# Kernel optimization log

Hardware: AMD Instinct MI355X
Metric: run time of the kernel (lower is better)

Reference implementation:

```python
import jax, jax.numpy as jnp
import numpy as np

GROUPS = 32
HEADS = 8
EPS = 1e-5

def setup_inputs() -> dict:
    key = jax.random.key(0)
    ks = jax.random.split(key, 5)
    C = 512
    x = jax.random.normal(ks[0], (8, C, 32, 32), dtype=jnp.float32)
    gn_w = jnp.ones((C,), dtype=jnp.float32)
    gn_b = jnp.zeros((C,), dtype=jnp.float32)
    qkv_w = jax.random.normal(ks[1], (3 * C, C), dtype=jnp.float32) * 0.02
    qkv_b = jnp.zeros((3 * C,), dtype=jnp.float32)
    proj_w = jax.random.normal(ks[2], (C, C), dtype=jnp.float32) * 0.02
    proj_b = jnp.zeros((C,), dtype=jnp.float32)
    return {"x": x, "gn_w": gn_w, "gn_b": gn_b, "qkv_w": qkv_w,
            "qkv_b": qkv_b, "proj_w": proj_w, "proj_b": proj_b}

def reference(x, gn_w, gn_b, qkv_w, qkv_b, proj_w, proj_b):
    B, C, H, W = x.shape
    d = C // HEADS
    # GroupNorm(32, C)
    xg = x.reshape(B, GROUPS, C // GROUPS, H, W)
    mean = xg.mean(axis=(2, 3, 4), keepdims=True)
    var = xg.var(axis=(2, 3, 4), keepdims=True)
    h = ((xg - mean) * jax.lax.rsqrt(var + EPS)).reshape(B, C, H, W)
    h = h * gn_w[None, :, None, None] + gn_b[None, :, None, None]
    # 1x1 conv QKV == channel matmul
    qkv = jnp.einsum('bchw,oc->bohw', h, qkv_w) + qkv_b[None, :, None, None]
    qkv = qkv.reshape(B, 3, HEADS, d, H * W)
    q, k, v = qkv[:, 0], qkv[:, 1], qkv[:, 2]  # [B, heads, d, HW]
    scale = d ** (-0.5)
    # weight[b,h,q,k] = sum_d q[b,h,d,q] * k[b,h,d,k] * scale
    attn = jax.nn.softmax(jnp.einsum('bhdq,bhdk->bhqk', q, k) * scale, axis=-1)
    # out[b,h,d,q] = sum_k v[b,h,d,k] * attn[b,h,q,k]
    out = jnp.einsum('bhdk,bhqk->bhdq', v, attn).reshape(B, C, H, W)
    out = jnp.einsum('bchw,oc->bohw', out, proj_w) + proj_b[None, :, None, None]
    return out + x
```

## Files before the change

kernel.cpp:

```cpp
#include <hip/hip_runtime.h>
#include <math.h>

#define B_    8
#define C_    512
#define HW_   1024
#define O3_   1536
#define HEADS_ 8
#define D_    64
#define G_    32
#define CPG_  16
#define EPS_  1e-5f
#define M_TOT 8192

#define QSCALE (0.125f * 1.44269504088896f)

typedef __bf16 bf16x8 __attribute__((ext_vector_type(8)));
typedef __bf16 bf16x4 __attribute__((ext_vector_type(4)));
typedef float  f32x4  __attribute__((ext_vector_type(4)));

__device__ __forceinline__ void async_copy16(void* lds, const void* g) {
  __builtin_amdgcn_global_load_lds(
      (const __attribute__((address_space(1))) unsigned int*)g,
      (__attribute__((address_space(3))) unsigned int*)lds, 16, 0, 0);
}

__global__ __launch_bounds__(1024) void k_gn(const float* __restrict__ x,
                                             const float* __restrict__ gw,
                                             const float* __restrict__ gb,
                                             __bf16* __restrict__ h,
                                             const float* __restrict__ qw,
                                             const float* __restrict__ pw,
                                             __bf16* __restrict__ qwb,
                                             __bf16* __restrict__ pwb) {
  __shared__ float red[34];
  __shared__ __bf16 T[16 * 1032];
  int tid = threadIdx.x;
  if (blockIdx.x >= B_ * G_) {
    int i0 = (blockIdx.x - B_ * G_) * 1024 + tid;
    for (int i = i0; i < O3_ * C_ / 4; i += 64 * 1024) {
      float4 v = ((const float4*)qw)[i];
      bf16x4 o = {(__bf16)v.x, (__bf16)v.y, (__bf16)v.z, (__bf16)v.w};
      ((bf16x4*)qwb)[i] = o;
    }
    for (int i = i0; i < C_ * C_ / 4; i += 64 * 1024) {
      float4 v = ((const float4*)pw)[i];
      bf16x4 o = {(__bf16)v.x, (__bf16)v.y, (__bf16)v.z, (__bf16)v.w};
      ((bf16x4*)pwb)[i] = o;
    }
    return;
  }
  int bg = blockIdx.x;
  int b = bg >> 5, g = bg & 31;
  const float4* xg4 = (const float4*)(x + ((size_t)(b * C_) + g * CPG_) * HW_);

  float s = 0.f, ss = 0.f;
  for (int i = tid; i < CPG_ * HW_ / 4; i += 1024) {
    float4 v = xg4[i];
    s += v.x + v.y + v.z + v.w;
    ss += v.x * v.x + v.y * v.y + v.z * v.z + v.w * v.w;
  }
  for (int off = 32; off > 0; off >>= 1) {
    s  += __shfl_down(s, off, 64);
    ss += __shfl_down(ss, off, 64);
  }
  int wv = tid >> 6;
  if ((tid & 63) == 0) { red[wv] = s; red[16 + wv] = ss; }
  __syncthreads();
  if (tid == 0) {
    float S = 0.f, SS = 0.f;
#pragma unroll
    for (int i = 0; i < 16; i++) { S += red[i]; SS += red[16 + i]; }
    float mean = S / (float)(CPG_ * HW_);
    float var  = SS / (float)(CPG_ * HW_) - mean * mean;
    red[32] = mean;
    red[33] = rsqrtf(var + EPS_);
  }
  __syncthreads();
  float mean = red[32], rstd = red[33];

  for (int i = tid; i < CPG_ * HW_ / 4; i += 1024) {
    int c = i >> 8;
    int hw4 = (i & 255) * 4;
    float ga = gw[g * CPG_ + c], be = gb[g * CPG_ + c];
    float4 v = xg4[i];
    bf16x4 pk;
    pk[0] = (__bf16)((v.x - mean) * rstd * ga + be);
    pk[1] = (__bf16)((v.y - mean) * rstd * ga + be);
    pk[2] = (__bf16)((v.z - mean) * rstd * ga + be);
    pk[3] = (__bf16)((v.w - mean) * rstd * ga + be);
    *(bf16x4*)(&T[c * 1032 + hw4]) = pk;
  }
  __syncthreads();

  __bf16* hb = h + (size_t)b * HW_ * C_ + g * CPG_;
  for (int j = tid; j < 2 * HW_; j += 1024) {
    int hw = j >> 1, c8 = (j & 1) * 8;
    bf16x8 v;
#pragma unroll
    for (int jj = 0; jj < 8; jj++) v[jj] = T[(c8 + jj) * 1032 + hw];
    *(bf16x8*)(hb + (size_t)hw * C_ + c8) = v;
  }
}

#define BKQ 32
__global__ __launch_bounds__(256, 3) void k_qkv(const __bf16* __restrict__ h,
                                                const __bf16* __restrict__ w,
                                                const float* __restrict__ bias,
                                                __bf16* __restrict__ y,
                                                __bf16* __restrict__ vT) {
  __shared__ __align__(16) __bf16 As[2][128 * BKQ];
  __shared__ __align__(16) __bf16 Bs[2][128 * BKQ];
  int m0 = blockIdx.x * 128, n0 = blockIdx.y * 128;
  int t = threadIdx.x;
  int lane = t & 63, l16 = lane & 15, quad = lane >> 4;
  int wv = t >> 6;
  int wm = (wv >> 1) * 64, wn = (wv & 1) * 64;

  int rsub = lane >> 2;
  int chunk = (lane & 3) ^ (rsub & 3);
  const __bf16* ag = h + (size_t)(m0 + wv * 32 + rsub) * C_ + chunk * 8;
  const __bf16* bg = w + (size_t)(n0 + wv * 32 + rsub) * C_ + chunk * 8;
  int sw = l16 & 3;

  auto stage = [&](int k0, int bi) {
    __bf16* la = As[bi] + wv * 1024 + lane * 8;
    __bf16* lb = Bs[bi] + wv * 1024 + lane * 8;
#pragma unroll
    for (int s = 0; s < 2; s++) {
      async_copy16(la + s * 512, ag + (size_t)(s * 16) * C_ + k0);
      async_copy16(lb + s * 512, bg + (size_t)(s * 16) * C_ + k0);
    }
  };

  f32x4 acc[4][4];
#pragma unroll
  for (int i = 0; i < 4; i++)
#pragma unroll
    for (int j = 0; j < 4; j++) acc[i][j] = f32x4{0.f, 0.f, 0.f, 0.f};

  stage(0, 0);
  stage(1 * BKQ, 1);
  for (int kk = 0; kk < 16; kk++) {
    int bi = kk & 1;
    if (kk < 15)
      asm volatile("s_waitcnt vmcnt(4)\n\ts_barrier" ::: "memory");
    else
      asm volatile("s_waitcnt vmcnt(0)\n\ts_barrier" ::: "memory");
    const __bf16* as = As[bi];
    const __bf16* bs = Bs[bi];
    bf16x8 af[4], bf[4];
#pragma unroll
    for (int i = 0; i < 4; i++) {
      af[i] = *(const bf16x8*)(as + (wm + i * 16 + l16) * BKQ + (quad ^ sw) * 8);
      bf[i] = *(const bf16x8*)(bs + (wn + i * 16 + l16) * BKQ + (quad ^ sw) * 8);
    }
    asm volatile("s_waitcnt lgkmcnt(0)\n\ts_barrier" ::: "memory");
    if (kk < 14) stage((kk + 2) * BKQ, bi);
    __builtin_amdgcn_s_setprio(1);
#pragma unroll
    for (int i = 0; i < 4; i++)
#pragma unroll
      for (int j = 0; j < 4; j++)
        acc[i][j] = __builtin_amdgcn_mfma_f32_16x16x32_bf16(af[i], bf[j],
                                                            acc[i][j], 0, 0, 0);
    __builtin_amdgcn_s_setprio(0);
  }

  if (n0 >= 2 * C_) {
    int bb = m0 >> 10;
    int tokBase = (m0 & 1023) + wm + quad * 4;
#pragma unroll
    for (int j = 0; j < 4; j++) {
      int n = n0 + wn + j * 16 + l16;
      int c = n - 2 * C_;
      float bv = bias[n];
      __bf16* vrow = vT + ((size_t)(bb * C_) + c) * HW_;
#pragma unroll
      for (int i = 0; i < 4; i++) {
        bf16x4 pk;
#pragma unroll
        for (int r = 0; r < 4; r++) pk[r] = (__bf16)(acc[i][j][r] + bv);
        *(bf16x4*)(vrow + tokBase + i * 16) = pk;
      }
    }
  } else {
    float sc = (n0 < C_) ? QSCALE : 1.0f;
#pragma unroll
    for (int j = 0; j < 4; j++) {
      int n = n0 + wn + j * 16 + l16;
      float bv = bias[n];
#pragma unroll
      for (int i = 0; i < 4; i++)
#pragma unroll
        for (int r = 0; r < 4; r++) {
          int m = m0 + wm + i * 16 + quad * 4 + r;
          y[(size_t)m * O3_ + n] = (__bf16)((acc[i][j][r] + bv) * sc);
        }
    }
  }
}

__global__ __launch_bounds__(256) void k_attn(const __bf16* __restrict__ y,
                                              const __bf16* __restrict__ vT,
                                              __bf16* __restrict__ ao) {
  __shared__ __align__(16) __bf16 Ks[2][128 * 64];
  __shared__ __align__(16) __bf16 Vt[2][64 * 128];
  __shared__ __align__(16) __bf16 Pp[4][32 * 36];
  int hd = blockIdx.x, b = blockIdx.y, qt = blockIdx.z;
  int t = threadIdx.x;
  int wv = t >> 6, lane = t & 63, l16 = lane & 15, quad = lane >> 4;
  int q0 = qt * 128 + wv * 32;

  const __bf16* base = y + (size_t)(b * HW_) * O3_ + hd * D_;
  const __bf16* kg = base + C_;
  const __bf16* vtg = vT + ((size_t)(b * C_) + hd * D_) * HW_;

  bf16x8 qb[2][2];
#pragma unroll
  for (int qg = 0; qg < 2; qg++)
#pragma unroll
    for (int dh = 0; dh < 2; dh++)
      qb[qg][dh] = *(const bf16x8*)(base + (size_t)(q0 + qg * 16 + l16) * O3_ +
                                    dh * 32 + quad * 8);

  int kRowSub = lane >> 3;
  int kChunk = (lane & 7) ^ (kRowSub & 7);

  auto stage = [&](int kt, int bi) {
#pragma unroll
    for (int s = 0; s < 4; s++) {
      int row = wv * 32 + s * 8 + kRowSub;
      async_copy16(&Ks[bi][(wv * 32 + s * 8) * 64 + lane * 8],
                   kg + (size_t)(kt + row) * O3_ + kChunk * 8);
    }
#pragma unroll
    for (int s = 0; s < 4; s++) {
      int row = wv * 16 + s * 4 + (lane >> 4);
      int c2 = (lane & 15) ^ (row & 15);
      async_copy16(&Vt[bi][(wv * 16 + s * 4) * 128 + lane * 8],
                   vtg + (size_t)row * HW_ + kt + c2 * 8);
    }
  };

  float l_run[2] = {0.f, 0.f};
  f32x4 o_acc[4][2];
#pragma unroll
  for (int dt = 0; dt < 4; dt++)
#pragma unroll
    for (int qg = 0; qg < 2; qg++) o_acc[dt][qg] = f32x4{0.f, 0.f, 0.f, 0.f};

  stage(0, 0);

  for (int step = 0; step < 8; step++) {
    int bi = step & 1;
    asm volatile("s_waitcnt vmcnt(0)\n\ts_barrier" ::: "memory");
    if (step < 7) stage((step + 1) * 128, bi ^ 1);

    const __bf16* ks = Ks[bi];
    const __bf16* vs = Vt[bi];
#pragma unroll
    for (int kh = 0; kh < 4; kh++) {
      f32x4 st[2][2];
      __builtin_amdgcn_s_setprio(1);
#pragma unroll
      for (int tti = 0; tti < 2; tti++) {
        int row = (kh * 2 + tti) * 16 + l16;
        bf16x8 ka0 = *(const bf16x8*)(&ks[row * 64 + ((quad) ^ (l16 & 7)) * 8]);
        bf16x8 ka1 = *(const bf16x8*)(&ks[row * 64 + ((4 + quad) ^ (l16 & 7)) * 8]);
        f32x4 z = {0.f, 0.f, 0.f, 0.f};
        st[tti][0] = __builtin_amdgcn_mfma_f32_16x16x32_bf16(ka0, qb[0][0], z, 0, 0, 0);
        st[tti][0] = __builtin_amdgcn_mfma_f32_16x16x32_bf16(ka1, qb[0][1], st[tti][0], 0, 0, 0);
        st[tti][1] = __builtin_amdgcn_mfma_f32_16x16x32_bf16(ka0, qb[1][0], z, 0, 0, 0);
        st[tti][1] = __builtin_amdgcn_mfma_f32_16x16x32_bf16(ka1, qb[1][1], st[tti][1], 0, 0, 0);
      }
      __builtin_amdgcn_s_setprio(0);
#pragma unroll
      for (int qg = 0; qg < 2; qg++) {
        float rs = 0.f;
#pragma unroll
        for (int tti = 0; tti < 2; tti++)
#pragma unroll
          for (int r = 0; r < 4; r++) {
            float e = __builtin_amdgcn_exp2f(st[tti][qg][r]);
            st[tti][qg][r] = e;
            rs += e;
          }
        l_run[qg] += rs;
      }
#pragma unroll
      for (int qg = 0; qg < 2; qg++)
#pragma unroll
        for (int tti = 0; tti < 2; tti++) {
          bf16x4 pk;
#pragma unroll
          for (int r = 0; r < 4; r++) pk[r] = (__bf16)st[tti][qg][r];
          *(bf16x4*)(&Pp[wv][(qg * 16 + l16) * 36 + tti * 16 + quad * 4]) = pk;
        }
      asm volatile("s_waitcnt lgkmcnt(0)" ::: "memory");
      bf16x8 pb0 = *(const bf16x8*)(&Pp[wv][l16 * 36 + quad * 8]);
      bf16x8 pb1 = *(const bf16x8*)(&Pp[wv][(16 + l16) * 36 + quad * 8]);
      __builtin_amdgcn_s_setprio(1);
#pragma unroll
      for (int dt = 0; dt < 4; dt++) {
        int vpos = ((kh * 4 + quad) ^ l16) * 8;
        bf16x8 va = *(const bf16x8*)(&vs[(dt * 16 + l16) * 128 + vpos]);
        o_acc[dt][0] = __builtin_amdgcn_mfma_f32_16x16x32_bf16(va, pb0, o_acc[dt][0], 0, 0, 0);
        o_acc[dt][1] = __builtin_amdgcn_mfma_f32_16x16x32_bf16(va, pb1, o_acc[dt][1], 0, 0, 0);
      }
      __builtin_amdgcn_s_setprio(0);
    }
  }

#pragma unroll
  for (int qg = 0; qg < 2; qg++) {
    l_run[qg] += __shfl_xor(l_run[qg], 16, 64);
    l_run[qg] += __shfl_xor(l_run[qg], 32, 64);
  }
  float inv0 = 1.f / l_run[0], inv1 = 1.f / l_run[1];

#pragma unroll
  for (int dt = 0; dt < 4; dt++) {
    bf16x4 p0, p1;
#pragma unroll
    for (int r = 0; r < 4; r++) {
      p0[r] = (__bf16)(o_acc[dt][0][r] * inv0);
      p1[r] = (__bf16)(o_acc[dt][1][r] * inv1);
    }
    int ch = hd * D_ + dt * 16 + quad * 4;
    *(bf16x4*)(ao + (size_t)(b * HW_ + q0 + l16) * C_ + ch) = p0;
    *(bf16x4*)(ao + (size_t)(b * HW_ + q0 + 16 + l16) * C_ + ch) = p1;
  }
}

#define BK 64
__global__ __launch_bounds__(256) void k_proj(const __bf16* __restrict__ ao,
                                              const __bf16* __restrict__ w,
                                              const float* __restrict__ bias,
                                              const float* __restrict__ x,
                                              float* __restrict__ out) {
  __shared__ __align__(16) __bf16 As[2][128 * BK];
  __shared__ __align__(16) __bf16 Bs[2][64 * BK];
  int n0 = blockIdx.x * 64, m0 = blockIdx.y * 128;
  int t = threadIdx.x;
  int lane = t & 63, l16 = lane & 15, quad = lane >> 4;
  int wv = t >> 6;
  int wm = (wv >> 1) * 64, wn = (wv & 1) * 32;

  int rsub = lane >> 3;
  int chunk = (lane & 7) ^ rsub;
  const __bf16* ag = w + (size_t)(m0 + wv * 32 + rsub) * C_ + chunk * 8;
  const __bf16* bg = ao + (size_t)(n0 + wv * 16 + rsub) * C_ + chunk * 8;
  int sw = l16 & 7;

  auto stage = [&](int k0, int bi) {
    __bf16* la = As[bi] + wv * 2048 + lane * 8;
    __bf16* lb = Bs[bi] + wv * 1024 + lane * 8;
#pragma unroll
    for (int s = 0; s < 4; s++)
      async_copy16(la + s * 512, ag + (size_t)(s * 8) * C_ + k0);
#pragma unroll
    for (int s = 0; s < 2; s++)
      async_copy16(lb + s * 512, bg + (size_t)(s * 8) * C_ + k0);
  };

  f32x4 acc[4][2];
#pragma unroll
  for (int i = 0; i < 4; i++)
#pragma unroll
    for (int j = 0; j < 2; j++) acc[i][j] = f32x4{0.f, 0.f, 0.f, 0.f};

  stage(0, 0);
  stage(1 * BK, 1);
  for (int kk = 0; kk < 8; kk++) {
    int bi = kk & 1;
    if (kk < 7)
      asm volatile("s_waitcnt vmcnt(6)\n\ts_barrier" ::: "memory");
    else
      asm volatile("s_waitcnt vmcnt(0)\n\ts_barrier" ::: "memory");
    const __bf16* as = As[bi];
    const __bf16* bs = Bs[bi];
    bf16x8 af[2][4], bf[2][2];
#pragma unroll
    for (int hh = 0; hh < 2; hh++) {
#pragma unroll
      for (int i = 0; i < 4; i++)
        af[hh][i] = *(const bf16x8*)(as + (wm + i * 16 + l16) * BK +
                                     ((hh * 4 + quad) ^ sw) * 8);
#pragma unroll
      for (int j = 0; j < 2; j++)
        bf[hh][j] = *(const bf16x8*)(bs + (wn + j * 16 + l16) * BK +
                                     ((hh * 4 + quad) ^ sw) * 8);
    }
    asm volatile("s_waitcnt lgkmcnt(0)\n\ts_barrier" ::: "memory");
    if (kk < 6) stage((kk + 2) * BK, bi);
    __builtin_amdgcn_s_setprio(1);
#pragma unroll
    for (int hh = 0; hh < 2; hh++)
#pragma unroll
      for (int i = 0; i < 4; i++)
#pragma unroll
        for (int j = 0; j < 2; j++)
          acc[i][j] = __builtin_amdgcn_mfma_f32_16x16x32_bf16(af[hh][i], bf[hh][j],
                                                              acc[i][j], 0, 0, 0);
    __builtin_amdgcn_s_setprio(0);
  }

  int bb = n0 >> 10;
#pragma unroll
  for (int i = 0; i < 4; i++)
#pragma unroll
    for (int r = 0; r < 4; r++) {
      int o = m0 + wm + i * 16 + quad * 4 + r;
      float bv = bias[o];
#pragma unroll
      for (int j = 0; j < 2; j++) {
        int n = n0 + wn + j * 16 + l16;
        int hw = n & 1023;
        size_t idx = ((size_t)(bb * C_ + o)) * HW_ + hw;
        out[idx] = acc[i][j][r] + bv + x[idx];
      }
    }
}

extern "C" void kernel_launch(void* const* d_in, const int* in_sizes, int n_in,
                              void* d_out, int out_size, void* d_ws, size_t ws_size,
                              hipStream_t stream) {
  const float* x      = (const float*)d_in[0];
  const float* gn_w   = (const float*)d_in[1];
  const float* gn_b   = (const float*)d_in[2];
  const float* qkv_w  = (const float*)d_in[3];
  const float* qkv_b  = (const float*)d_in[4];
  const float* proj_w = (const float*)d_in[5];
  const float* proj_b = (const float*)d_in[6];
  float* out = (float*)d_out;

  char* ws = (char*)d_ws;
  __bf16* h   = (__bf16*)(ws);
  __bf16* qwb = (__bf16*)(ws + 8388608);
  __bf16* pwb = (__bf16*)(ws + 8388608 + 1572864);
  __bf16* yq  = (__bf16*)(ws + 8388608 + 1572864 + 524288);
  __bf16* ao  = (__bf16*)(ws + 8388608 + 1572864 + 524288 + 25165824);
  __bf16* vT  = (__bf16*)(ws + 8388608 + 1572864 + 524288 + 25165824 + 8388608);

  k_gn  <<<B_ * G_ + 64, 1024, 0, stream>>>(x, gn_w, gn_b, h,
                                            qkv_w, proj_w, qwb, pwb);
  k_qkv <<<dim3(M_TOT / 128, O3_ / 128, 1), 256, 0, stream>>>(h, qwb, qkv_b, yq, vT);
  k_attn<<<dim3(HEADS_, B_, 8), 256, 0, stream>>>(yq, vT, ao);
  k_proj<<<dim3(M_TOT / 64, C_ / 128, 1), 256, 0, stream>>>(ao, pwb, proj_b, x, out);
  (void)in_sizes; (void)n_in; (void)out_size; (void)ws_size;
}
```

Baseline: 141.7 us.

## Enlarge QKV GEMM tiles to 256x256 with BK=64 and 8 waves

Rewrites the QKV projection GEMM to use 256x256 block tiles with 512 threads and a K-step of 64, using an 8-wide XOR swizzle and split LDS fragment loads inside each step. Each wave now computes a 128x64 subtile, which raises arithmetic intensity per LDS/global load and halves the number of barrier iterations. The trade-off is far fewer blocks (192 vs 768), which may underfill the GPU's CUs, plus higher register and LDS pressure (128KB LDS double-buffered).

```diff
diff --git a/kernel.cpp b/kernel.cpp
--- a/kernel.cpp
+++ b/kernel.cpp
@@ -102,66 +102,84 @@
   }
 }
 
-#define BKQ 32
-__global__ __launch_bounds__(256, 3) void k_qkv(const __bf16* __restrict__ h,
+#define BKW 64
+__global__ __launch_bounds__(512, 2) void k_qkv(const __bf16* __restrict__ h,
                                                 const __bf16* __restrict__ w,
                                                 const float* __restrict__ bias,
                                                 __bf16* __restrict__ y,
                                                 __bf16* __restrict__ vT) {
-  __shared__ __align__(16) __bf16 As[2][128 * BKQ];
-  __shared__ __align__(16) __bf16 Bs[2][128 * BKQ];
-  int m0 = blockIdx.x * 128, n0 = blockIdx.y * 128;
+  __shared__ __align__(16) __bf16 As[2][256 * BKW];
+  __shared__ __align__(16) __bf16 Bs[2][256 * BKW];
+  int m0 = blockIdx.x * 256, n0 = blockIdx.y * 256;
   int t = threadIdx.x;
   int lane = t & 63, l16 = lane & 15, quad = lane >> 4;
   int wv = t >> 6;
-  int wm = (wv >> 1) * 64, wn = (wv & 1) * 64;
-
-  int rsub = lane >> 2;
-  int chunk = (lane & 3) ^ (rsub & 3);
+  int wm = (wv >> 2) * 128, wn = (wv & 3) * 64;
+
+  int rsub = lane >> 3;
+  int chunk = (lane & 7) ^ rsub;
   const __bf16* ag = h + (size_t)(m0 + wv * 32 + rsub) * C_ + chunk * 8;
   const __bf16* bg = w + (size_t)(n0 + wv * 32 + rsub) * C_ + chunk * 8;
-  int sw = l16 & 3;
+  int sw = l16 & 7;
 
   auto stage = [&](int k0, int bi) {
-    __bf16* la = As[bi] + wv * 1024 + lane * 8;
-    __bf16* lb = Bs[bi] + wv * 1024 + lane * 8;
-#pragma unroll
-    for (int s = 0; s < 2; s++) {
-      async_copy16(la + s * 512, ag + (size_t)(s * 16) * C_ + k0);
-      async_copy16(lb + s * 512, bg + (size_t)(s * 16) * C_ + k0);
+    __bf16* la = As[bi] + wv * 32 * BKW + lane * 8;
+    __bf16* lb = Bs[bi] + wv * 32 * BKW + lane * 8;
+#pragma unroll
+    for (int s = 0; s < 4; s++) {
+      async_copy16(la + s * 8 * BKW, ag + (size_t)(s * 8) * C_ + k0);
+      async_copy16(lb + s * 8 * BKW, bg + (size_t)(s * 8) * C_ + k0);
     }
   };
 
-  f32x4 acc[4][4];
-#pragma unroll
-  for (int i = 0; i < 4; i++)
+  f32x4 acc[8][4];
+#pragma unroll
+  for (int i = 0; i < 8; i++)
 #pragma unroll
     for (int j = 0; j < 4; j++) acc[i][j] = f32x4{0.f, 0.f, 0.f, 0.f};
 
   stage(0, 0);
-  stage(1 * BKQ, 1);
-  for (int kk = 0; kk < 16; kk++) {
+  stage(BKW, 1);
+  for (int kk = 0; kk < 8; kk++) {
     int bi = kk & 1;
-    if (kk < 15)
-      asm volatile("s_waitcnt vmcnt(4)\n\ts_barrier" ::: "memory");
+    if (kk < 7)
+      asm volatile("s_waitcnt vmcnt(8)\n\ts_barrier" ::: "memory");
     else
       asm volatile("s_waitcnt vmcnt(0)\n\ts_barrier" ::: "memory");
     const __bf16* as = As[bi];
     const __bf16* bs = Bs[bi];
-    bf16x8 af[4], bf[4];
-#pragma unroll
-    for (int i = 0; i < 4; i++) {
-      af[i] = *(const bf16x8*)(as + (wm + i * 16 + l16) * BKQ + (quad ^ sw) * 8);
-      bf[i] = *(const bf16x8*)(bs + (wn + i * 16 + l16) * BKQ + (quad ^ sw) * 8);
-    }
+
+    bf16x8 af[8], bfr[4];
+#pragma unroll
+    for (int i = 0; i < 8; i++)
+      af[i] = *(const bf16x8*)(as + (wm + i * 16 + l16) * BKW + (quad ^ sw) * 8);
+#pragma unroll
+    for (int j = 0; j < 4; j++)
+      bfr[j] = *(const bf16x8*)(bs + (wn + j * 16 + l16) * BKW + (quad ^ sw) * 8);
+    __builtin_amdgcn_s_setprio(1);
+#pragma unroll
+    for (int i = 0; i < 8; i++)
+#pragma unroll
+      for (int j = 0; j < 4; j++)
+        acc[i][j] = __builtin_amdgcn_mfma_f32_16x16x32_bf16(af[i], bfr[j],
+                                                            acc[i][j], 0, 0, 0);
+    __builtin_amdgcn_s_setprio(0);
+#pragma unroll
+    for (int i = 0; i < 8; i++)
+      af[i] = *(const bf16x8*)(as + (wm + i * 16 + l16) * BKW +
+                               ((4 + quad) ^ sw) * 8);
+#pragma unroll
+    for (int j = 0; j < 4; j++)
+      bfr[j] = *(const bf16x8*)(bs + (wn + j * 16 + l16) * BKW +
+                                ((4 + quad) ^ sw) * 8);
     asm volatile("s_waitcnt lgkmcnt(0)\n\ts_barrier" ::: "memory");
-    if (kk < 14) stage((kk + 2) * BKQ, bi);
+    if (kk < 6) stage((kk + 2) * BKW, bi);
     __builtin_amdgcn_s_setprio(1);
 #pragma unroll
-    for (int i = 0; i < 4; i++)
+    for (int i = 0; i < 8; i++)
 #pragma unroll
       for (int j = 0; j < 4; j++)
-        acc[i][j] = __builtin_amdgcn_mfma_f32_16x16x32_bf16(af[i], bf[j],
+        acc[i][j] = __builtin_amdgcn_mfma_f32_16x16x32_bf16(af[i], bfr[j],
                                                             acc[i][j], 0, 0, 0);
     __builtin_amdgcn_s_setprio(0);
   }
@@ -176,7 +194,7 @@
       float bv = bias[n];
       __bf16* vrow = vT + ((size_t)(bb * C_) + c) * HW_;
 #pragma unroll
-      for (int i = 0; i < 4; i++) {
+      for (int i = 0; i < 8; i++) {
         bf16x4 pk;
 #pragma unroll
         for (int r = 0; r < 4; r++) pk[r] = (__bf16)(acc[i][j][r] + bv);
@@ -190,7 +208,7 @@
       int n = n0 + wn + j * 16 + l16;
       float bv = bias[n];
 #pragma unroll
-      for (int i = 0; i < 4; i++)
+      for (int i = 0; i < 8; i++)
 #pragma unroll
         for (int r = 0; r < 4; r++) {
           int m = m0 + wm + i * 16 + quad * 4 + r;
@@ -444,7 +462,7 @@
 
   k_gn  <<<B_ * G_ + 64, 1024, 0, stream>>>(x, gn_w, gn_b, h,
                                             qkv_w, proj_w, qwb, pwb);
-  k_qkv <<<dim3(M_TOT / 128, O3_ / 128, 1), 256, 0, stream>>>(h, qwb, qkv_b, yq, vT);
+  k_qkv <<<dim3(M_TOT / 256, O3_ / 256, 1), 512, 0, stream>>>(h, qwb, qkv_b, yq, vT);
   k_attn<<<dim3(HEADS_, B_, 8), 256, 0, stream>>>(yq, vT, ao);
   k_proj<<<dim3(M_TOT / 64, C_ / 128, 1), 256, 0, stream>>>(ao, pwb, proj_b, x, out);
   (void)in_sizes; (void)n_in; (void)out_size; (void)ws_size;
```

New measurement: 143.3 us. No clear change (+1.1%).

## Load K/V directly from global into registers in attention, halve query tile

Applied to the files above, without the earlier changes.

The attention kernel no longer stages K and V tiles in LDS with async copies and block barriers. Each wave now loads its K and V fragments straight from global memory into registers, double-buffering K across 32-key steps. Each wave handles 16 queries instead of 32, so the grid doubles to 16 query tiles per head. This removes LDS traffic and barriers and should raise occupancy, but each block reads K/V from global/L2 with no sharing across waves, which multiplies L2 traffic and adds latency exposure.

```diff
diff --git a/kernel.cpp b/kernel.cpp
--- a/kernel.cpp
+++ b/kernel.cpp
@@ -203,132 +203,93 @@
 __global__ __launch_bounds__(256) void k_attn(const __bf16* __restrict__ y,
                                               const __bf16* __restrict__ vT,
                                               __bf16* __restrict__ ao) {
-  __shared__ __align__(16) __bf16 Ks[2][128 * 64];
-  __shared__ __align__(16) __bf16 Vt[2][64 * 128];
-  __shared__ __align__(16) __bf16 Pp[4][32 * 36];
+  __shared__ __align__(16) __bf16 Pp[4][16 * 36];
   int hd = blockIdx.x, b = blockIdx.y, qt = blockIdx.z;
   int t = threadIdx.x;
   int wv = t >> 6, lane = t & 63, l16 = lane & 15, quad = lane >> 4;
-  int q0 = qt * 128 + wv * 32;
+  int q0 = qt * 64 + wv * 16;
 
   const __bf16* base = y + (size_t)(b * HW_) * O3_ + hd * D_;
-  const __bf16* kg = base + C_;
   const __bf16* vtg = vT + ((size_t)(b * C_) + hd * D_) * HW_;
 
-  bf16x8 qb[2][2];
-#pragma unroll
-  for (int qg = 0; qg < 2; qg++)
-#pragma unroll
-    for (int dh = 0; dh < 2; dh++)
-      qb[qg][dh] = *(const bf16x8*)(base + (size_t)(q0 + qg * 16 + l16) * O3_ +
-                                    dh * 32 + quad * 8);
-
-  int kRowSub = lane >> 3;
-  int kChunk = (lane & 7) ^ (kRowSub & 7);
-
-  auto stage = [&](int kt, int bi) {
-#pragma unroll
-    for (int s = 0; s < 4; s++) {
-      int row = wv * 32 + s * 8 + kRowSub;
-      async_copy16(&Ks[bi][(wv * 32 + s * 8) * 64 + lane * 8],
-                   kg + (size_t)(kt + row) * O3_ + kChunk * 8);
-    }
-#pragma unroll
-    for (int s = 0; s < 4; s++) {
-      int row = wv * 16 + s * 4 + (lane >> 4);
-      int c2 = (lane & 15) ^ (row & 15);
-      async_copy16(&Vt[bi][(wv * 16 + s * 4) * 128 + lane * 8],
-                   vtg + (size_t)row * HW_ + kt + c2 * 8);
-    }
+  bf16x8 qb[2];
+#pragma unroll
+  for (int dh = 0; dh < 2; dh++)
+    qb[dh] = *(const bf16x8*)(base + (size_t)(q0 + l16) * O3_ +
+                              dh * 32 + quad * 8);
+
+  const __bf16* kL = base + C_ + (size_t)l16 * O3_ + quad * 8;
+  const __bf16* vL = vtg + (size_t)l16 * HW_ + quad * 8;
+
+  float l_run = 0.f;
+  f32x4 o_acc[4];
+#pragma unroll
+  for (int dt = 0; dt < 4; dt++) o_acc[dt] = f32x4{0.f, 0.f, 0.f, 0.f};
+
+  bf16x8 kaE[2][2], kaO[2][2], va[4];
+
+  auto LK = [&](bf16x8 (&dst)[2][2], int s) {
+#pragma unroll
+    for (int tti = 0; tti < 2; tti++)
+#pragma unroll
+      for (int dh = 0; dh < 2; dh++)
+        dst[tti][dh] = *(const bf16x8*)(kL + (size_t)(s * 32 + tti * 16) * O3_ +
+                                        dh * 32);
   };
-
-  float l_run[2] = {0.f, 0.f};
-  f32x4 o_acc[4][2];
-#pragma unroll
-  for (int dt = 0; dt < 4; dt++)
-#pragma unroll
-    for (int qg = 0; qg < 2; qg++) o_acc[dt][qg] = f32x4{0.f, 0.f, 0.f, 0.f};
-
-  stage(0, 0);
-
-  for (int step = 0; step < 8; step++) {
-    int bi = step & 1;
-    asm volatile("s_waitcnt vmcnt(0)\n\ts_barrier" ::: "memory");
-    if (step < 7) stage((step + 1) * 128, bi ^ 1);
-
-    const __bf16* ks = Ks[bi];
-    const __bf16* vs = Vt[bi];
-#pragma unroll
-    for (int kh = 0; kh < 4; kh++) {
-      f32x4 st[2][2];
-      __builtin_amdgcn_s_setprio(1);
-#pragma unroll
-      for (int tti = 0; tti < 2; tti++) {
-        int row = (kh * 2 + tti) * 16 + l16;
-        bf16x8 ka0 = *(const bf16x8*)(&ks[row * 64 + ((quad) ^ (l16 & 7)) * 8]);
-        bf16x8 ka1 = *(const bf16x8*)(&ks[row * 64 + ((4 + quad) ^ (l16 & 7)) * 8]);
-        f32x4 z = {0.f, 0.f, 0.f, 0.f};
-        st[tti][0] = __builtin_amdgcn_mfma_f32_16x16x32_bf16(ka0, qb[0][0], z, 0, 0, 0);
-        st[tti][0] = __builtin_amdgcn_mfma_f32_16x16x32_bf16(ka1, qb[0][1], st[tti][0], 0, 0, 0);
-        st[tti][1] = __builtin_amdgcn_mfma_f32_16x16x32_bf16(ka0, qb[1][0], z, 0, 0, 0);
-        st[tti][1] = __builtin_amdgcn_mfma_f32_16x16x32_bf16(ka1, qb[1][1], st[tti][1], 0, 0, 0);
-      }
-      __builtin_amdgcn_s_setprio(0);
-#pragma unroll
-      for (int qg = 0; qg < 2; qg++) {
-        float rs = 0.f;
-#pragma unroll
-        for (int tti = 0; tti < 2; tti++)
-#pragma unroll
-          for (int r = 0; r < 4; r++) {
-            float e = __builtin_amdgcn_exp2f(st[tti][qg][r]);
-            st[tti][qg][r] = e;
-            rs += e;
-          }
-        l_run[qg] += rs;
-      }
-#pragma unroll
-      for (int qg = 0; qg < 2; qg++)
-#pragma unroll
-        for (int tti = 0; tti < 2; tti++) {
-          bf16x4 pk;
-#pragma unroll
-          for (int r = 0; r < 4; r++) pk[r] = (__bf16)st[tti][qg][r];
-          *(bf16x4*)(&Pp[wv][(qg * 16 + l16) * 36 + tti * 16 + quad * 4]) = pk;
-        }
-      asm volatile("s_waitcnt lgkmcnt(0)" ::: "memory");
-      bf16x8 pb0 = *(const bf16x8*)(&Pp[wv][l16 * 36 + quad * 8]);
-      bf16x8 pb1 = *(const bf16x8*)(&Pp[wv][(16 + l16) * 36 + quad * 8]);
-      __builtin_amdgcn_s_setprio(1);
-#pragma unroll
-      for (int dt = 0; dt < 4; dt++) {
-        int vpos = ((kh * 4 + quad) ^ l16) * 8;
-        bf16x8 va = *(const bf16x8*)(&vs[(dt * 16 + l16) * 128 + vpos]);
-        o_acc[dt][0] = __builtin_amdgcn_mfma_f32_16x16x32_bf16(va, pb0, o_acc[dt][0], 0, 0, 0);
-        o_acc[dt][1] = __builtin_amdgcn_mfma_f32_16x16x32_bf16(va, pb1, o_acc[dt][1], 0, 0, 0);
-      }
-      __builtin_amdgcn_s_setprio(0);
-    }
-  }
-
-#pragma unroll
-  for (int qg = 0; qg < 2; qg++) {
-    l_run[qg] += __shfl_xor(l_run[qg], 16, 64);
-    l_run[qg] += __shfl_xor(l_run[qg], 32, 64);
-  }
-  float inv0 = 1.f / l_run[0], inv1 = 1.f / l_run[1];
+  auto LV = [&](int s) {
+#pragma unroll
+    for (int dt = 0; dt < 4; dt++)
+      va[dt] = *(const bf16x8*)(vL + (size_t)(dt * 16) * HW_ + s * 32);
+  };
+  auto BODY = [&](bf16x8 (&ka)[2][2]) {
+    f32x4 z = {0.f, 0.f, 0.f, 0.f};
+    __builtin_amdgcn_s_setprio(1);
+    f32x4 st0 = __builtin_amdgcn_mfma_f32_16x16x32_bf16(ka[0][0], qb[0], z, 0, 0, 0);
+    st0 = __builtin_amdgcn_mfma_f32_16x16x32_bf16(ka[0][1], qb[1], st0, 0, 0, 0);
+    f32x4 st1 = __builtin_amdgcn_mfma_f32_16x16x32_bf16(ka[1][0], qb[0], z, 0, 0, 0);
+    st1 = __builtin_amdgcn_mfma_f32_16x16x32_bf16(ka[1][1], qb[1], st1, 0, 0, 0);
+    __builtin_amdgcn_s_setprio(0);
+    float rs = 0.f;
+    bf16x4 p0, p1;
+#pragma unroll
+    for (int r = 0; r < 4; r++) {
+      float e0 = __builtin_amdgcn_exp2f(st0[r]); rs += e0; p0[r] = (__bf16)e0;
+      float e1 = __builtin_amdgcn_exp2f(st1[r]); rs += e1; p1[r] = (__bf16)e1;
+    }
+    l_run += rs;
+    *(bf16x4*)(&Pp[wv][l16 * 36 + quad * 4]) = p0;
+    *(bf16x4*)(&Pp[wv][l16 * 36 + 16 + quad * 4]) = p1;
+    asm volatile("s_waitcnt lgkmcnt(0)" ::: "memory");
+    bf16x8 pb = *(const bf16x8*)(&Pp[wv][l16 * 36 + quad * 8]);
+    __builtin_amdgcn_s_setprio(1);
+#pragma unroll
+    for (int dt = 0; dt < 4; dt++)
+      o_acc[dt] = __builtin_amdgcn_mfma_f32_16x16x32_bf16(va[dt], pb,
+                                                          o_acc[dt], 0, 0, 0);
+    __builtin_amdgcn_s_setprio(0);
+  };
+
+  LK(kaE, 0);
+  for (int s = 0; s < 32; s += 2) {
+    LV(s);
+    LK(kaO, s + 1);
+    BODY(kaE);
+    LV(s + 1);
+    if (s + 2 < 32) LK(kaE, s + 2);
+    BODY(kaO);
+  }
+
+  l_run += __shfl_xor(l_run, 16, 64);
+  l_run += __shfl_xor(l_run, 32, 64);
+  float inv = 1.f / l_run;
 
 #pragma unroll
   for (int dt = 0; dt < 4; dt++) {
-    bf16x4 p0, p1;
-#pragma unroll
-    for (int r = 0; r < 4; r++) {
-      p0[r] = (__bf16)(o_acc[dt][0][r] * inv0);
-      p1[r] = (__bf16)(o_acc[dt][1][r] * inv1);
-    }
+    bf16x4 pk;
+#pragma unroll
+    for (int r = 0; r < 4; r++) pk[r] = (__bf16)(o_acc[dt][r] * inv);
     int ch = hd * D_ + dt * 16 + quad * 4;
-    *(bf16x4*)(ao + (size_t)(b * HW_ + q0 + l16) * C_ + ch) = p0;
-    *(bf16x4*)(ao + (size_t)(b * HW_ + q0 + 16 + l16) * C_ + ch) = p1;
+    *(bf16x4*)(ao + (size_t)(b * HW_ + q0 + l16) * C_ + ch) = pk;
   }
 }
 
@@ -445,7 +406,7 @@
   k_gn  <<<B_ * G_ + 64, 1024, 0, stream>>>(x, gn_w, gn_b, h,
                                             qkv_w, proj_w, qwb, pwb);
   k_qkv <<<dim3(M_TOT / 128, O3_ / 128, 1), 256, 0, stream>>>(h, qwb, qkv_b, yq, vT);
-  k_attn<<<dim3(HEADS_, B_, 8), 256, 0, stream>>>(yq, vT, ao);
+  k_attn<<<dim3(HEADS_, B_, 16), 256, 0, stream>>>(yq, vT, ao);
   k_proj<<<dim3(M_TOT / 64, C_ / 128, 1), 256, 0, stream>>>(ao, pwb, proj_b, x, out);
   (void)in_sizes; (void)n_in; (void)out_size; (void)ws_size;
 }
```

Measured after the change: 228.1 us. 1.61x slower.
